# Kernel optimization log

Hardware: AMD Instinct MI355X
Metric: run time of the kernel (lower is better)

## Reference

```python
import jax, jax.numpy as jnp
import numpy as np

N = 50000      # num_nodes
E = 800000     # num_edges
D = 128        # hidden_dim
POOL_RATIO = 0.5
CROSS_W = 1.0  # cross_weight


def _gcn(x, W, b, src, dst, n):
    """GCNConv: symmetric-normalized aggregation with self-loops. Dropout is identity (eval)."""
    loops = jnp.arange(n)
    s = jnp.concatenate([src, loops])
    d = jnp.concatenate([dst, loops])
    deg = jax.ops.segment_sum(jnp.ones(s.shape, x.dtype), d, num_segments=n)
    inv_sqrt = jax.lax.rsqrt(jnp.maximum(deg, 1.0))  # deg >= 1 due to self-loops
    xw = x @ W                                        # [n, D]
    msg = xw[s] * (inv_sqrt[s] * inv_sqrt[d])[:, None]  # [E+n, D] gather
    return jax.ops.segment_sum(msg, d, num_segments=n) + b


def _prelu(x, a):
    return jnp.where(x >= 0, x, a * x)


def setup_inputs() -> dict:
    key = jax.random.key(0)
    ks = jax.random.split(key, 8)
    glorot = lambda k, sh: jax.random.normal(k, sh, jnp.float32) * np.float32(np.sqrt(2.0 / (sh[0] + sh[1])))
    return {
        "feat": jax.random.normal(ks[0], (N, D), jnp.float32),
        "h_neg": jax.random.normal(ks[1], (N, D), jnp.float32),
        "edge_index": jax.random.randint(ks[2], (2, E), 0, N),
        "Wd": glorot(ks[3], (D, D)),
        "bd": jnp.zeros((D,), jnp.float32),
        "prelu_a": jnp.full((1,), 0.25, jnp.float32),
        "Wbil": glorot(ks[4], (D, D)),
        "bbil": jnp.zeros((1,), jnp.float32),
        "Wg1": glorot(ks[5], (D, D)),
        "bg1": jnp.zeros((D,), jnp.float32),
        "Wg2": glorot(ks[6], (D, D)),
        "bg2": jnp.zeros((D,), jnp.float32),
        "Wg3": glorot(ks[7], (D, D)),
        "bg3": jnp.zeros((D,), jnp.float32),
    }


def reference(feat, h_neg, edge_index, Wd, bd, prelu_a, Wbil, bbil,
              Wg1, bg1, Wg2, bg2, Wg3, bg3):
    src, dst = edge_index[0], edge_index[1]
    # --- IndexSelect: dense layer on pos/neg features ---
    h_pos = _prelu(feat @ Wd + bd, prelu_a)
    h_neg_d = _prelu(h_neg @ Wd + bd, prelu_a)
    embed = _gcn(h_pos, Wg1, bg1, src, dst, N)
    h_center = jax.nn.sigmoid(embed)
    # Discriminator (bilinear) positive scores -> node importance
    score_pos = jnp.einsum('nd,de,ne->n', h_pos, Wbil, h_center) + bbil[0]
    _ = jnp.einsum('nd,de,ne->n', h_neg_d, Wbil, h_center) + bbil[0]  # score_neg (logits branch)
    scores = jax.nn.sigmoid(score_pos)
    order = jnp.argsort(-scores)           # descending
    k = int(POOL_RATIO * N)
    select_idx = order[:k]
    select_scores = scores[order][:k]
    # --- GraphPool (use_gcn=True): down-sample GCN, gather, scale ---
    pooled = _gcn(embed, Wg2, bg2, src, dst, N)[select_idx] * select_scores[:, None]
    # --- GraphUnpool: scatter into zeros, up-sample GCN ---
    fine = jnp.zeros((N, D), feat.dtype).at[select_idx].set(pooled)
    out = _gcn(fine, Wg3, bg3, src, dst, N)
    # --- cross/fuse connection ---
    return out + CROSS_W * embed
```

## Files before the change

### kernel.cpp

```cpp
#include <hip/hip_runtime.h>
#include <hip/hip_bf16.h>

#define NN 50000
#define NE 800000
#define DD 128
#define KSEL 25000
#define NBK 391
#define NBLKA 98
#define AB 12500

typedef unsigned int uint32;
typedef unsigned short ushort16;
typedef __attribute__((ext_vector_type(8))) short bf16x8;
typedef __attribute__((ext_vector_type(4))) float f32x4;

__device__ __forceinline__ float sigmoidf(float x){ return 1.f/(1.f+__expf(-x)); }

__device__ __forceinline__ unsigned short f2b(float f){
  union{float f; unsigned u;} v; v.f=f;
  unsigned r=(v.u + 0x7fffu + ((v.u>>16)&1u))>>16;
  return (unsigned short)r;
}

__device__ __forceinline__ void addbf2(float&lo,float&hi,uint32 u,float w){
  lo+=__uint_as_float(u<<16)*w;
  hi+=__uint_as_float(u&0xffff0000u)*w;
}

__device__ __forceinline__ int aload(const int* p){
  return __hip_atomic_load(p,__ATOMIC_RELAXED,__HIP_MEMORY_SCOPE_AGENT);
}

__global__ __launch_bounds__(256) void k_prep(const float* __restrict__ Wbil,
    float* __restrict__ WbT, const float* __restrict__ Wg2, ushort16* __restrict__ Wt2b,
    const float* __restrict__ Wg3, ushort16* __restrict__ Wt3b,
    int* __restrict__ zspan, int* __restrict__ btot){
  int i=blockIdx.x*256+threadIdx.x;
  if(i<DD*DD){
    int n=i>>7, k=i&127;
    WbT[i]=Wbil[k*DD+n];
    Wt2b[i]=f2b(Wg2[(size_t)k*DD+n]);
    Wt3b[i]=f2b(Wg3[(size_t)k*DD+n]);
  }
  if(i<8512) zspan[i]=0;
  if(i<NBK) btot[i]=0;
}

__global__ __launch_bounds__(1024) void k_bcount(const int* __restrict__ dst,
    int* __restrict__ btot, int* __restrict__ blkcnt){
  __shared__ int h[NBK];
  int tid=threadIdx.x;
  for(int i=tid;i<NBK;i+=1024) h[i]=0;
  __syncthreads();
  int e0=blockIdx.x*8192;
  #pragma unroll
  for(int t=0;t<8;t++){
    int e=e0+t*1024+tid;
    if(e<NE) atomicAdd(&h[dst[e]>>7],1);
  }
  __syncthreads();
  for(int i=tid;i<NBK;i+=1024){
    int c=h[i];
    blkcnt[blockIdx.x*NBK+i]=c;
    if(c) atomicAdd(&btot[i],c);
  }
}

__global__ __launch_bounds__(512) void k_bscan(const int* __restrict__ btot,
    int* __restrict__ boff, const int* __restrict__ blkcnt, int* __restrict__ blkbase,
    int* __restrict__ row_start){
  __shared__ int sdata[512];
  int tid=threadIdx.x;
  int v=(tid<NBK)?btot[tid]:0;
  sdata[tid]=v; __syncthreads();
  for(int off=1;off<512;off<<=1){
    int y=(tid>=off)?sdata[tid-off]:0;
    __syncthreads();
    sdata[tid]+=y;
    __syncthreads();
  }
  int excl=sdata[tid]-v;
  if(tid<NBK) boff[tid]=excl;
  if(tid==NBK-1){ boff[NBK]=excl+v; row_start[NN]=NE; }
  if(tid<NBK){
    int run=excl;
    for(int b=0;b<NBLKA;b++){
      int c=blkcnt[b*NBK+tid];
      blkbase[b*NBK+tid]=run;
      run+=c;
    }
  }
}

__global__ __launch_bounds__(1024) void k_bscatter(const int* __restrict__ src,
    const int* __restrict__ dst, const int* __restrict__ blkbase, uint32* __restrict__ pairs){
  __shared__ int cur[NBK];
  int tid=threadIdx.x;
  for(int i=tid;i<NBK;i+=1024) cur[i]=blkbase[blockIdx.x*NBK+i];
  __syncthreads();
  int e0=blockIdx.x*8192;
  #pragma unroll
  for(int t=0;t<8;t++){
    int e=e0+t*1024+tid;
    if(e<NE){
      int d=dst[e];
      int p=atomicAdd(&cur[d>>7],1);
      pairs[p]=(unsigned)src[e] | ((unsigned)(d&127)<<17);
    }
  }
}

__global__ __launch_bounds__(256) void k_bfinal(const uint32* __restrict__ pairs,
    const int* __restrict__ boff, int* __restrict__ row_start,
    float* __restrict__ inv_sq, int* __restrict__ csr_src){
  __shared__ int degl[128];
  __shared__ int cur[128];
  __shared__ int ssum[2];
  int b=blockIdx.x, tid=threadIdx.x;
  int lo=boff[b], hi=boff[b+1];
  if(tid<128) degl[tid]=0;
  __syncthreads();
  for(int e=lo+tid;e<hi;e+=256) atomicAdd(&degl[pairs[e]>>17],1);
  __syncthreads();
  int v=0,x=0;
  if(tid<128){
    v=degl[tid]; x=v;
    #pragma unroll
    for(int off=1;off<64;off<<=1){
      int y=__shfl_up(x,off,64);
      if((tid&63)>=off) x+=y;
    }
    if((tid&63)==63) ssum[tid>>6]=x;
  }
  __syncthreads();
  if(tid<128){
    int incl=x+((tid>=64)?ssum[0]:0);
    int node=b*128+tid;
    int excl=lo+incl-v;
    if(node<NN){
      row_start[node]=excl;
      cur[tid]=excl;
      inv_sq[node]=1.f/sqrtf((float)(v+1));
    }
  }
  __syncthreads();
  for(int e=lo+tid;e<hi;e+=256){
    uint32 u=pairs[e];
    int p=atomicAdd(&cur[u>>17],1);
    csr_src[p]=(int)(u&0x1FFFFu);
  }
}

template<int IN_SIG,int ACT,int FUSE_SCORE>
__global__ __launch_bounds__(256) void k_gemm64t(const float* __restrict__ A,
    const float* __restrict__ W, const float* __restrict__ bias,
    float* __restrict__ outf,
    const float* __restrict__ aparam, const float* __restrict__ hp,
    const float* __restrict__ bbil, float* __restrict__ score){
  __shared__ float Al[64][132];
  int tid=threadIdx.x;
  int row0=blockIdx.x*64;
  {
    const float4* A4=(const float4*)(A+(size_t)row0*DD);
    #pragma unroll
    for(int i=0;i<8;i++){
      int idx=i*256+tid;
      int r=idx>>5, c=(idx&31)*4;
      float4 v=make_float4(0.f,0.f,0.f,0.f);
      if(row0+r<NN) v=A4[idx];
      if(IN_SIG){ v.x=sigmoidf(v.x); v.y=sigmoidf(v.y); v.z=sigmoidf(v.z); v.w=sigmoidf(v.w); }
      *(float4*)&Al[r][c]=v;
    }
  }
  __syncthreads();
  int tx=tid&31, ty=tid>>5;
  float acc[8][4];
  #pragma unroll
  for(int i=0;i<8;i++)
    #pragma unroll
    for(int c=0;c<4;c++) acc[i][c]=0.f;

  for(int k=0;k<DD;k+=4){
    float4 wv0=*(const float4*)&W[(size_t)(k+0)*DD+tx*4];
    float4 wv1=*(const float4*)&W[(size_t)(k+1)*DD+tx*4];
    float4 wv2=*(const float4*)&W[(size_t)(k+2)*DD+tx*4];
    float4 wv3=*(const float4*)&W[(size_t)(k+3)*DD+tx*4];
    #pragma unroll
    for(int i=0;i<8;i++){
      float4 a=*(const float4*)&Al[ty+8*i][k];
      acc[i][0]+=a.x*wv0.x+a.y*wv1.x+a.z*wv2.x+a.w*wv3.x;
      acc[i][1]+=a.x*wv0.y+a.y*wv1.y+a.z*wv2.y+a.w*wv3.y;
      acc[i][2]+=a.x*wv0.z+a.y*wv1.z+a.z*wv2.z+a.w*wv3.z;
      acc[i][3]+=a.x*wv0.w+a.y*wv1.w+a.z*wv2.w+a.w*wv3.w;
    }
  }

  if(FUSE_SCORE){
    float bb=bbil[0];
    #pragma unroll
    for(int i=0;i<8;i++){
      int r=row0+ty+8*i;
      float p=0.f;
      if(r<NN){
        float4 h=*(const float4*)&hp[(size_t)r*DD+tx*4];
        p=acc[i][0]*h.x+acc[i][1]*h.y+acc[i][2]*h.z+acc[i][3]*h.w;
      }
      p+=__shfl_xor(p,16,64); p+=__shfl_xor(p,8,64);
      p+=__shfl_xor(p,4,64);  p+=__shfl_xor(p,2,64); p+=__shfl_xor(p,1,64);
      if(tx==0 && r<NN) score[r]=sigmoidf(p+bb);
    }
    return;
  }
  float4 bv=make_float4(0.f,0.f,0.f,0.f);
  if(bias) bv=*(const float4*)&bias[tx*4];
  float ap=ACT?aparam[0]:0.f;
  #pragma unroll
  for(int i=0;i<8;i++){
    int r=row0+ty+8*i;
    if(r<NN){
      float4 o;
      o.x=acc[i][0]+bv.x; o.y=acc[i][1]+bv.y; o.z=acc[i][2]+bv.z; o.w=acc[i][3]+bv.w;
      if(ACT){
        o.x=o.x>=0.f?o.x:ap*o.x; o.y=o.y>=0.f?o.y:ap*o.y;
        o.z=o.z>=0.f?o.z:ap*o.z; o.w=o.w>=0.f?o.w:ap*o.w;
      }
      *(float4*)&outf[(size_t)r*DD+tx*4]=o;
    }
  }
}

template<int ROWLIST>
__global__ __launch_bounds__(256) void k_gemm_mfma(const float* __restrict__ A,
    const ushort16* __restrict__ Wtb, ushort16* __restrict__ outb,
    const int* __restrict__ rlist){
  __shared__ __align__(16) unsigned short Asl[64][136];
  __shared__ __align__(16) unsigned short Wsl[128][136];
  int tid=threadIdx.x;
  int row0=blockIdx.x*64;
  {
    const uint4* Wg=(const uint4*)Wtb;
    #pragma unroll
    for(int i=0;i<8;i++){
      int idx=i*256+tid;
      int n=idx>>4, k8=(idx&15)*8;
      uint4 v=Wg[idx];
      *(uint4*)&Wsl[n][k8]=v;
    }
  }
  {
    #pragma unroll
    for(int i=0;i<8;i++){
      int idx=i*256+tid;
      int r=idx>>5, c=(idx&31)*4;
      int gr; bool ok;
      if(ROWLIST){ int ri=row0+r; ok=(ri<KSEL); gr=ok?rlist[ri]:0; }
      else { gr=row0+r; ok=(gr<NN); }
      float4 v=make_float4(0.f,0.f,0.f,0.f);
      if(ok) v=*(const float4*)&A[(size_t)gr*DD+c];
      ushort4 pk;
      pk.x=f2b(v.x); pk.y=f2b(v.y); pk.z=f2b(v.z); pk.w=f2b(v.w);
      *(ushort4*)&Asl[r][c]=pk;
    }
  }
  __syncthreads();
  int lane=tid&63, w=tid>>6;
  int lr=lane&15, lk=lane>>4;
  f32x4 acc[8];
  #pragma unroll
  for(int nf=0;nf<8;nf++){ acc[nf][0]=0.f; acc[nf][1]=0.f; acc[nf][2]=0.f; acc[nf][3]=0.f; }
  #pragma unroll
  for(int kk=0;kk<4;kk++){
    int k0=kk*32+lk*8;
    bf16x8 a=*(bf16x8*)&Asl[w*16+lr][k0];
    #pragma unroll
    for(int nf=0;nf<8;nf++){
      bf16x8 b=*(bf16x8*)&Wsl[nf*16+lr][k0];
      acc[nf]=__builtin_amdgcn_mfma_f32_16x16x32_bf16(a,b,acc[nf],0,0,0);
    }
  }
  int orow[4]; bool ok[4];
  #pragma unroll
  for(int i=0;i<4;i++){
    int ri=row0+w*16+lk*4+i;
    if(ROWLIST){ ok[i]=(ri<KSEL); orow[i]=ok[i]?rlist[ri]:0; }
    else { orow[i]=ri; ok[i]=(ri<NN); }
  }
  #pragma unroll
  for(int nf=0;nf<8;nf++){
    int col=nf*16+lr;
    #pragma unroll
    for(int i=0;i<4;i++){
      if(ok[i]) outb[(size_t)orow[i]*DD+col]=f2b(acc[nf][i]);
    }
  }
}

__global__ __launch_bounds__(256) void k_agg_f32(const float* __restrict__ xw,
    const int* __restrict__ row_start, const int* __restrict__ csr,
    const float* __restrict__ inv, const float* __restrict__ bias,
    float* __restrict__ outp){
  int node=blockIdx.x*4+(threadIdx.x>>6);
  if(node>=NN) return;
  int lane=threadIdx.x&63;
  int g=lane>>5, li=lane&31;
  int rs=row_start[node], re=row_start[node+1];
  float a0=0.f,a1=0.f,a2=0.f,a3=0.f;
  int j=rs;
  for(; j+7<re; j+=8){
    int s0=csr[j+g], s1=csr[j+2+g], s2=csr[j+4+g], s3=csr[j+6+g];
    float w0=inv[s0], w1=inv[s1], w2=inv[s2], w3=inv[s3];
    float4 v0=*(const float4*)&xw[(size_t)s0*DD+li*4];
    float4 v1=*(const float4*)&xw[(size_t)s1*DD+li*4];
    float4 v2=*(const float4*)&xw[(size_t)s2*DD+li*4];
    float4 v3=*(const float4*)&xw[(size_t)s3*DD+li*4];
    a0+=v0.x*w0+v1.x*w1+v2.x*w2+v3.x*w3;
    a1+=v0.y*w0+v1.y*w1+v2.y*w2+v3.y*w3;
    a2+=v0.z*w0+v1.z*w1+v2.z*w2+v3.z*w3;
    a3+=v0.w*w0+v1.w*w1+v2.w*w2+v3.w*w3;
  }
  for(; j+1<re; j+=2){
    int s=csr[j+g];
    float w=inv[s];
    float4 v=*(const float4*)&xw[(size_t)s*DD+li*4];
    a0+=v.x*w; a1+=v.y*w; a2+=v.z*w; a3+=v.w*w;
  }
  if(j<re && g==0){
    int s=csr[j]; float w=inv[s];
    float4 v=*(const float4*)&xw[(size_t)s*DD+li*4];
    a0+=v.x*w; a1+=v.y*w; a2+=v.z*w; a3+=v.w*w;
  }
  if(g==0){
    float wd=inv[node];
    float4 v=*(const float4*)&xw[(size_t)node*DD+li*4];
    a0+=v.x*wd; a1+=v.y*wd; a2+=v.z*wd; a3+=v.w*wd;
  }
  a0+=__shfl_xor(a0,32,64); a1+=__shfl_xor(a1,32,64);
  a2+=__shfl_xor(a2,32,64); a3+=__shfl_xor(a3,32,64);
  if(g==0){
    float wn=inv[node];
    float4 bv=*(const float4*)&bias[li*4];
    float4 o;
    o.x=a0*wn+bv.x; o.y=a1*wn+bv.y; o.z=a2*wn+bv.z; o.w=a3*wn+bv.w;
    *(float4*)&outp[(size_t)node*DD+li*4]=o;
  }
}

template<int MODE>
__global__ __launch_bounds__(256) void k_agg_b16(const uint32* __restrict__ xwb,
    const int* __restrict__ row_start, const int* __restrict__ csr,
    const float* __restrict__ inv, const float* __restrict__ bias,
    float* __restrict__ outp, const float* __restrict__ score,
    const unsigned char* __restrict__ sel, const float* __restrict__ addbuf,
    const int* __restrict__ list){
  int idx4=blockIdx.x*4+(threadIdx.x>>6);
  int node;
  if(MODE==1){ if(idx4>=KSEL) return; node=list[idx4]; }
  else { node=idx4; if(node>=NN) return; }
  int lane=threadIdx.x&63;
  int g=lane>>4, li=lane&15;
  int rs=row_start[node], re=row_start[node+1];
  float a[8];
  #pragma unroll
  for(int c=0;c<8;c++) a[c]=0.f;
  int j=rs;
  for(; j+7<re; j+=8){
    int sA=csr[j+g], sB=csr[j+4+g];
    if(MODE!=2 || sel[sA]){
      float w=inv[sA];
      uint4 u=*(const uint4*)(xwb+(size_t)sA*64+li*4);
      addbf2(a[0],a[1],u.x,w); addbf2(a[2],a[3],u.y,w);
      addbf2(a[4],a[5],u.z,w); addbf2(a[6],a[7],u.w,w);
    }
    if(MODE!=2 || sel[sB]){
      float w=inv[sB];
      uint4 u=*(const uint4*)(xwb+(size_t)sB*64+li*4);
      addbf2(a[0],a[1],u.x,w); addbf2(a[2],a[3],u.y,w);
      addbf2(a[4],a[5],u.z,w); addbf2(a[6],a[7],u.w,w);
    }
  }
  for(; j+3<re; j+=4){
    int s=csr[j+g];
    if(MODE!=2 || sel[s]){
      float w=inv[s];
      uint4 u=*(const uint4*)(xwb+(size_t)s*64+li*4);
      addbf2(a[0],a[1],u.x,w); addbf2(a[2],a[3],u.y,w);
      addbf2(a[4],a[5],u.z,w); addbf2(a[6],a[7],u.w,w);
    }
  }
  int rem=re-j;
  if(g<rem){
    int s=csr[j+g];
    if(MODE!=2 || sel[s]){
      float w=inv[s];
      uint4 u=*(const uint4*)(xwb+(size_t)s*64+li*4);
      addbf2(a[0],a[1],u.x,w); addbf2(a[2],a[3],u.y,w);
      addbf2(a[4],a[5],u.z,w); addbf2(a[6],a[7],u.w,w);
    }
  }
  if(g==0 && (MODE!=2 || sel[node])){
    float wd=inv[node];
    uint4 u=*(const uint4*)(xwb+(size_t)node*64+li*4);
    addbf2(a[0],a[1],u.x,wd); addbf2(a[2],a[3],u.y,wd);
    addbf2(a[4],a[5],u.z,wd); addbf2(a[6],a[7],u.w,wd);
  }
  #pragma unroll
  for(int c=0;c<8;c++){
    a[c]+=__shfl_xor(a[c],16,64);
    a[c]+=__shfl_xor(a[c],32,64);
  }
  if(g<2){
    float wn=inv[node];
    int cb=li*8+g*4;
    float4 bv=*(const float4*)&bias[cb];
    float r0=a[g*4+0]*wn+bv.x, r1=a[g*4+1]*wn+bv.y;
    float r2=a[g*4+2]*wn+bv.z, r3=a[g*4+3]*wn+bv.w;
    if(MODE==1){
      float sc=score[node];
      r0*=sc; r1*=sc; r2*=sc; r3*=sc;
    } else {
      float4 ad=*(const float4*)&addbuf[(size_t)node*DD+cb];
      r0+=ad.x; r1+=ad.y; r2+=ad.z; r3+=ad.w;
    }
    float4 o; o.x=r0; o.y=r1; o.z=r2; o.w=r3;
    *(float4*)&outp[(size_t)node*DD+cb]=o;
  }
}

template<int NB,int PASS>
__global__ __launch_bounds__(256) void k_hist(const float* __restrict__ score,
    int* __restrict__ ghist, int* __restrict__ ctrl){
  __shared__ int lh[NB];
  __shared__ int gs[256];
  __shared__ int lastf;
  int tid=threadIdx.x;
  for(int i=tid;i<NB;i+=256) lh[i]=0;
  __syncthreads();
  int p0=0,p01=0;
  if(PASS==1) p0=ctrl[0];
  if(PASS==2) p01=ctrl[2];
  for(int i=blockIdx.x*256+tid; i<NN; i+=gridDim.x*256){
    unsigned b=__float_as_uint(score[i]);
    if(PASS==0) atomicAdd(&lh[b>>20],1);
    else if(PASS==1){ if((int)(b>>20)==p0) atomicAdd(&lh[(b>>8)&0xFFF],1); }
    else { if((int)(b>>8)==p01) atomicAdd(&lh[b&0xFF],1); }
  }
  __syncthreads();
  for(int i=tid;i<NB;i+=256){ int v=lh[i]; if(v) atomicAdd(&ghist[i],v); }
  __syncthreads();
  if(tid==0){
    __threadfence();
    int v=atomicAdd(&ctrl[8+PASS],1);
    lastf=(v==(int)gridDim.x-1);
  }
  __syncthreads();
  if(!lastf) return;
  const int BPT=NB/256;
  int s=0;
  #pragma unroll
  for(int q=0;q<BPT;q++) s+=aload(&ghist[tid*BPT+q]);
  int x=s; gs[tid]=x; __syncthreads();
  for(int off=1;off<256;off<<=1){
    int y=(tid+off<256)?gs[tid+off]:0;
    __syncthreads(); x+=y; gs[tid]=x; __syncthreads();
  }
  int base;
  if(PASS==0) base=0; else if(PASS==1) base=ctrl[1]; else base=ctrl[3];
  int above=base+x-s, incl=base+x;
  if(above<KSEL && incl>=KSEL){
    int c=above, B=0;
    for(int b=BPT-1;b>=0;b--){
      int hb=aload(&ghist[tid*BPT+b]);
      if(c+hb>=KSEL){ B=tid*BPT+b; break; }
      c+=hb;
    }
    if(PASS==0){ ctrl[0]=B; ctrl[1]=c; }
    else if(PASS==1){ ctrl[2]=(ctrl[0]<<12)|B; ctrl[3]=c; }
    else { ctrl[4]=(int)((((unsigned)ctrl[2])<<8)|(unsigned)B); ctrl[5]=KSEL-c; }
  }
}

__global__ __launch_bounds__(256) void k_sel(const float* __restrict__ score,
    int* __restrict__ ctrl, int* __restrict__ tie_list,
    unsigned char* __restrict__ sel, int* __restrict__ list){
  __shared__ int lastf;
  int tid=threadIdx.x;
  int i=blockIdx.x*256+tid;
  if(i<NN){
    unsigned b=__float_as_uint(score[i]);
    unsigned thr=(unsigned)ctrl[4];
    if(b>thr){
      sel[i]=1;
      int p=atomicAdd(&ctrl[7],1);
      list[p]=i;
    } else if(b==thr){
      sel[i]=0;
      int p=atomicAdd(&ctrl[6],1);
      if(p<4096) __hip_atomic_store(&tie_list[p],i,__ATOMIC_RELAXED,__HIP_MEMORY_SCOPE_AGENT);
    } else sel[i]=0;
  }
  __syncthreads();
  if(tid==0){
    __threadfence();
    int v=atomicAdd(&ctrl[11],1);
    lastf=(v==(int)gridDim.x-1);
  }
  __syncthreads();
  if(!lastf) return;
  int m=aload(&ctrl[6]); if(m>4096) m=4096;
  int needed=ctrl[5];
  for(int t=tid;t<m;t+=256){
    int idx=aload(&tie_list[t]);
    int rank=0;
    for(int j2=0;j2<m;j2++) rank+=(aload(&tie_list[j2])<idx)?1:0;
    if(rank<needed){
      sel[idx]=1;
      int p=atomicAdd(&ctrl[7],1);
      list[p]=idx;
    }
  }
}

extern "C" void kernel_launch(void* const* d_in, const int* in_sizes, int n_in,
                              void* d_out, int out_size, void* d_ws, size_t ws_size,
                              hipStream_t stream){
  const float* feat   =(const float*)d_in[0];
  const int*   ei     =(const int*)  d_in[2];
  const int*   src    = ei;
  const int*   dst    = ei + NE;
  const float* Wd     =(const float*)d_in[3];
  const float* bd     =(const float*)d_in[4];
  const float* prelu_a=(const float*)d_in[5];
  const float* Wbil   =(const float*)d_in[6];
  const float* bbil   =(const float*)d_in[7];
  const float* Wg1    =(const float*)d_in[8];
  const float* bg1    =(const float*)d_in[9];
  const float* Wg2    =(const float*)d_in[10];
  const float* bg2    =(const float*)d_in[11];
  const float* Wg3    =(const float*)d_in[12];
  const float* bg3    =(const float*)d_in[13];
  float* out=(float*)d_out;

  char* p=(char*)d_ws;
  auto alloc=[&](size_t bytes)->void*{ void* r=(void*)p; p+=((bytes+255)/256)*256; return r; };
  float* h_pos   =(float*)alloc((size_t)NN*DD*4);
  float* embed   =(float*)alloc((size_t)NN*DD*4);
  float* xw      =(float*)alloc((size_t)NN*DD*4);
  float* score   =(float*)alloc((size_t)NN*4);
  float* inv_sq  =(float*)alloc((size_t)NN*4);
  float* WbT     =(float*)alloc((size_t)DD*DD*4);
  ushort16* Wt2b =(ushort16*)alloc((size_t)DD*DD*2);
  ushort16* Wt3b =(ushort16*)alloc((size_t)DD*DD*2);
  int*   row_st  =(int*)  alloc((size_t)(NN+1)*4);
  int*   csr_src =(int*)  alloc((size_t)NE*4);
  int*   ctrl    =(int*)  alloc(256);
  int*   hist0   =(int*)  alloc(4096*4);
  int*   hist1   =(int*)  alloc(4096*4);
  int*   hist2   =(int*)  alloc(256*4);
  int*   tie_list=(int*)  alloc(4096*4);
  int*   list    =(int*)  alloc((size_t)KSEL*4);
  unsigned char* sel=(unsigned char*)alloc(NN);
  int*   btot    =(int*)  alloc((size_t)NBK*4);
  int*   boff    =(int*)  alloc((size_t)(NBK+1)*4);
  int*   blkcnt  =(int*)  alloc((size_t)NBLKA*NBK*4);
  int*   blkbase =(int*)  alloc((size_t)NBLKA*NBK*4);
  uint32* pairs  =(uint32*)xw;
  ushort16* xwb  =(ushort16*)xw;
  float* fine = out;

  const int NB=(NN+255)/256;
  const int GB=(NN+63)/64;
  const int GBL=(KSEL+63)/64;
  const int ABL=(KSEL+3)/4;

  k_prep<<<64,256,0,stream>>>(Wbil, WbT, Wg2, Wt2b, Wg3, Wt3b, ctrl, btot);

  k_bcount  <<<NBLKA,1024,0,stream>>>(dst, btot, blkcnt);
  k_bscan   <<<1,512,0,stream>>>(btot, boff, blkcnt, blkbase, row_st);
  k_bscatter<<<NBLKA,1024,0,stream>>>(src, dst, blkbase, pairs);
  k_bfinal  <<<NBK,256,0,stream>>>(pairs, boff, row_st, inv_sq, csr_src);

  k_gemm64t<0,1,0><<<GB,256,0,stream>>>(feat, Wd, bd, h_pos, prelu_a, nullptr, nullptr, nullptr);
  k_gemm64t<0,0,0><<<GB,256,0,stream>>>(h_pos, Wg1, nullptr, xw, nullptr, nullptr, nullptr, nullptr);
  k_agg_f32<<<AB,256,0,stream>>>(xw, row_st, csr_src, inv_sq, bg1, embed);
  k_gemm64t<1,0,1><<<GB,256,0,stream>>>(embed, WbT, nullptr, nullptr, nullptr, h_pos, bbil, score);
  k_hist<4096,0><<<64,256,0,stream>>>(score, hist0, ctrl);
  k_hist<4096,1><<<64,256,0,stream>>>(score, hist1, ctrl);
  k_hist<256,2><<<64,256,0,stream>>>(score, hist2, ctrl);
  k_sel<<<NB,256,0,stream>>>(score, ctrl, tie_list, sel, list);
  k_gemm_mfma<0><<<GB,256,0,stream>>>(embed, Wt2b, xwb, nullptr);
  k_agg_b16<1><<<ABL,256,0,stream>>>((const uint32*)xwb, row_st, csr_src, inv_sq, bg2, fine, score, sel, nullptr, list);
  k_gemm_mfma<1><<<GBL,256,0,stream>>>(fine, Wt3b, xwb, list);
  k_agg_b16<2><<<AB,256,0,stream>>>((const uint32*)xwb, row_st, csr_src, inv_sq, bg3, out, nullptr, sel, embed, nullptr);
}
```

Measured before the change: 330.0 us.

## Pack independent kernels into shared launches to cut launch count

Merges independent work into single heterogeneous launches by block index: the dense layer, the CSR bucket count and the weight prep share one grid, the Wg1 GEMM shares a grid with the bucket scan, and the Wg2 MFMA GEMM shares a grid with the first score-histogram pass. This is meant to cut kernel-launch and tail idle time on a mostly serial chain of small kernels and to let latency-bound CSR work overlap the GEMMs. The bucket-count grid is widened to more smaller blocks, and the scan becomes a single block with long serial loops over many block counts, which may end up on the critical path. The pairs buffer moves from xw to embed so the scatter does not clash with the concurrent GEMM output.

```diff
diff --git a/kernel.cpp b/kernel.cpp
--- a/kernel.cpp
+++ b/kernel.cpp
@@ -6,8 +6,11 @@
 #define DD 128
 #define KSEL 25000
 #define NBK 391
-#define NBLKA 98
+#define BC  391
 #define AB 12500
+#define GB 782
+#define GBL 391
+#define HB 64
 
 typedef unsigned int uint32;
 typedef unsigned short ushort16;
@@ -31,135 +34,11 @@
   return __hip_atomic_load(p,__ATOMIC_RELAXED,__HIP_MEMORY_SCOPE_AGENT);
 }
 
-__global__ __launch_bounds__(256) void k_prep(const float* __restrict__ Wbil,
-    float* __restrict__ WbT, const float* __restrict__ Wg2, ushort16* __restrict__ Wt2b,
-    const float* __restrict__ Wg3, ushort16* __restrict__ Wt3b,
-    int* __restrict__ zspan, int* __restrict__ btot){
-  int i=blockIdx.x*256+threadIdx.x;
-  if(i<DD*DD){
-    int n=i>>7, k=i&127;
-    WbT[i]=Wbil[k*DD+n];
-    Wt2b[i]=f2b(Wg2[(size_t)k*DD+n]);
-    Wt3b[i]=f2b(Wg3[(size_t)k*DD+n]);
-  }
-  if(i<8512) zspan[i]=0;
-  if(i<NBK) btot[i]=0;
-}
-
-__global__ __launch_bounds__(1024) void k_bcount(const int* __restrict__ dst,
-    int* __restrict__ btot, int* __restrict__ blkcnt){
-  __shared__ int h[NBK];
-  int tid=threadIdx.x;
-  for(int i=tid;i<NBK;i+=1024) h[i]=0;
-  __syncthreads();
-  int e0=blockIdx.x*8192;
-  #pragma unroll
-  for(int t=0;t<8;t++){
-    int e=e0+t*1024+tid;
-    if(e<NE) atomicAdd(&h[dst[e]>>7],1);
-  }
-  __syncthreads();
-  for(int i=tid;i<NBK;i+=1024){
-    int c=h[i];
-    blkcnt[blockIdx.x*NBK+i]=c;
-    if(c) atomicAdd(&btot[i],c);
-  }
-}
-
-__global__ __launch_bounds__(512) void k_bscan(const int* __restrict__ btot,
-    int* __restrict__ boff, const int* __restrict__ blkcnt, int* __restrict__ blkbase,
-    int* __restrict__ row_start){
-  __shared__ int sdata[512];
-  int tid=threadIdx.x;
-  int v=(tid<NBK)?btot[tid]:0;
-  sdata[tid]=v; __syncthreads();
-  for(int off=1;off<512;off<<=1){
-    int y=(tid>=off)?sdata[tid-off]:0;
-    __syncthreads();
-    sdata[tid]+=y;
-    __syncthreads();
-  }
-  int excl=sdata[tid]-v;
-  if(tid<NBK) boff[tid]=excl;
-  if(tid==NBK-1){ boff[NBK]=excl+v; row_start[NN]=NE; }
-  if(tid<NBK){
-    int run=excl;
-    for(int b=0;b<NBLKA;b++){
-      int c=blkcnt[b*NBK+tid];
-      blkbase[b*NBK+tid]=run;
-      run+=c;
-    }
-  }
-}
-
-__global__ __launch_bounds__(1024) void k_bscatter(const int* __restrict__ src,
-    const int* __restrict__ dst, const int* __restrict__ blkbase, uint32* __restrict__ pairs){
-  __shared__ int cur[NBK];
-  int tid=threadIdx.x;
-  for(int i=tid;i<NBK;i+=1024) cur[i]=blkbase[blockIdx.x*NBK+i];
-  __syncthreads();
-  int e0=blockIdx.x*8192;
-  #pragma unroll
-  for(int t=0;t<8;t++){
-    int e=e0+t*1024+tid;
-    if(e<NE){
-      int d=dst[e];
-      int p=atomicAdd(&cur[d>>7],1);
-      pairs[p]=(unsigned)src[e] | ((unsigned)(d&127)<<17);
-    }
-  }
-}
-
-__global__ __launch_bounds__(256) void k_bfinal(const uint32* __restrict__ pairs,
-    const int* __restrict__ boff, int* __restrict__ row_start,
-    float* __restrict__ inv_sq, int* __restrict__ csr_src){
-  __shared__ int degl[128];
-  __shared__ int cur[128];
-  __shared__ int ssum[2];
-  int b=blockIdx.x, tid=threadIdx.x;
-  int lo=boff[b], hi=boff[b+1];
-  if(tid<128) degl[tid]=0;
-  __syncthreads();
-  for(int e=lo+tid;e<hi;e+=256) atomicAdd(&degl[pairs[e]>>17],1);
-  __syncthreads();
-  int v=0,x=0;
-  if(tid<128){
-    v=degl[tid]; x=v;
-    #pragma unroll
-    for(int off=1;off<64;off<<=1){
-      int y=__shfl_up(x,off,64);
-      if((tid&63)>=off) x+=y;
-    }
-    if((tid&63)==63) ssum[tid>>6]=x;
-  }
-  __syncthreads();
-  if(tid<128){
-    int incl=x+((tid>=64)?ssum[0]:0);
-    int node=b*128+tid;
-    int excl=lo+incl-v;
-    if(node<NN){
-      row_start[node]=excl;
-      cur[tid]=excl;
-      inv_sq[node]=1.f/sqrtf((float)(v+1));
-    }
-  }
-  __syncthreads();
-  for(int e=lo+tid;e<hi;e+=256){
-    uint32 u=pairs[e];
-    int p=atomicAdd(&cur[u>>17],1);
-    csr_src[p]=(int)(u&0x1FFFFu);
-  }
-}
-
-template<int IN_SIG,int ACT,int FUSE_SCORE>
-__global__ __launch_bounds__(256) void k_gemm64t(const float* __restrict__ A,
-    const float* __restrict__ W, const float* __restrict__ bias,
-    float* __restrict__ outf,
-    const float* __restrict__ aparam, const float* __restrict__ hp,
-    const float* __restrict__ bbil, float* __restrict__ score){
-  __shared__ float Al[64][132];
-  int tid=threadIdx.x;
-  int row0=blockIdx.x*64;
+template<int IN_SIG,int ACT>
+__device__ __forceinline__ void gemm64_body(float (*Al)[132], int tid, int row0,
+    const float* __restrict__ A, const float* __restrict__ W,
+    const float* __restrict__ bias, float* __restrict__ outf,
+    const float* __restrict__ aparam){
   {
     const float4* A4=(const float4*)(A+(size_t)row0*DD);
     #pragma unroll
@@ -179,7 +58,6 @@
   for(int i=0;i<8;i++)
     #pragma unroll
     for(int c=0;c<4;c++) acc[i][c]=0.f;
-
   for(int k=0;k<DD;k+=4){
     float4 wv0=*(const float4*)&W[(size_t)(k+0)*DD+tx*4];
     float4 wv1=*(const float4*)&W[(size_t)(k+1)*DD+tx*4];
@@ -193,23 +71,6 @@
       acc[i][2]+=a.x*wv0.z+a.y*wv1.z+a.z*wv2.z+a.w*wv3.z;
       acc[i][3]+=a.x*wv0.w+a.y*wv1.w+a.z*wv2.w+a.w*wv3.w;
     }
-  }
-
-  if(FUSE_SCORE){
-    float bb=bbil[0];
-    #pragma unroll
-    for(int i=0;i<8;i++){
-      int r=row0+ty+8*i;
-      float p=0.f;
-      if(r<NN){
-        float4 h=*(const float4*)&hp[(size_t)r*DD+tx*4];
-        p=acc[i][0]*h.x+acc[i][1]*h.y+acc[i][2]*h.z+acc[i][3]*h.w;
-      }
-      p+=__shfl_xor(p,16,64); p+=__shfl_xor(p,8,64);
-      p+=__shfl_xor(p,4,64);  p+=__shfl_xor(p,2,64); p+=__shfl_xor(p,1,64);
-      if(tx==0 && r<NN) score[r]=sigmoidf(p+bb);
-    }
-    return;
   }
   float4 bv=make_float4(0.f,0.f,0.f,0.f);
   if(bias) bv=*(const float4*)&bias[tx*4];
@@ -230,13 +91,10 @@
 }
 
 template<int ROWLIST>
-__global__ __launch_bounds__(256) void k_gemm_mfma(const float* __restrict__ A,
-    const ushort16* __restrict__ Wtb, ushort16* __restrict__ outb,
-    const int* __restrict__ rlist){
-  __shared__ __align__(16) unsigned short Asl[64][136];
-  __shared__ __align__(16) unsigned short Wsl[128][136];
-  int tid=threadIdx.x;
-  int row0=blockIdx.x*64;
+__device__ __forceinline__ void mfma_body(unsigned short (*Asl)[136],
+    unsigned short (*Wsl)[136], int tid, int row0,
+    const float* __restrict__ A, const ushort16* __restrict__ Wtb,
+    ushort16* __restrict__ outb, const int* __restrict__ rlist){
   {
     const uint4* Wg=(const uint4*)Wtb;
     #pragma unroll
@@ -293,6 +151,356 @@
       if(ok[i]) outb[(size_t)orow[i]*DD+col]=f2b(acc[nf][i]);
     }
   }
+}
+
+__global__ __launch_bounds__(256) void k_pack1(
+    const float* __restrict__ feat, const float* __restrict__ Wd,
+    const float* __restrict__ bd, float* __restrict__ h_pos,
+    const float* __restrict__ aparam,
+    const int* __restrict__ dst, int* __restrict__ blkcnt,
+    const float* __restrict__ Wbil, float* __restrict__ WbT,
+    const float* __restrict__ Wg2, ushort16* __restrict__ Wt2b,
+    const float* __restrict__ Wg3, ushort16* __restrict__ Wt3b,
+    int* __restrict__ zspan){
+  __shared__ float Al[64][132];
+  int bid=blockIdx.x, tid=threadIdx.x;
+  if(bid<GB){
+    gemm64_body<0,1>(Al, tid, bid*64, feat, Wd, bd, h_pos, aparam);
+    return;
+  }
+  if(bid<GB+BC){
+    int b=bid-GB;
+    int* h=(int*)Al;
+    for(int i=tid;i<NBK;i+=256) h[i]=0;
+    __syncthreads();
+    int e0=b*2048;
+    #pragma unroll
+    for(int t=0;t<8;t++){
+      int e=e0+t*256+tid;
+      if(e<NE) atomicAdd(&h[dst[e]>>7],1);
+    }
+    __syncthreads();
+    for(int i=tid;i<NBK;i+=256) blkcnt[b*NBK+i]=h[i];
+    return;
+  }
+  int i=(bid-GB-BC)*256+tid;
+  if(i<DD*DD){
+    int n=i>>7, k=i&127;
+    WbT[i]=Wbil[k*DD+n];
+    Wt2b[i]=f2b(Wg2[(size_t)k*DD+n]);
+    Wt3b[i]=f2b(Wg3[(size_t)k*DD+n]);
+  }
+  if(i<8512) zspan[i]=0;
+}
+
+__global__ __launch_bounds__(256) void k_pack2(
+    const float* __restrict__ h_pos, const float* __restrict__ Wg1,
+    float* __restrict__ xw,
+    const int* __restrict__ blkcnt, int* __restrict__ boff,
+    int* __restrict__ blkbase, int* __restrict__ row_start){
+  __shared__ float Al[64][132];
+  int bid=blockIdx.x, tid=threadIdx.x;
+  if(bid<GB){
+    gemm64_body<0,0>(Al, tid, bid*64, h_pos, Wg1, nullptr, xw, nullptr);
+    return;
+  }
+  int* sd=(int*)Al;
+  int b0=tid, b1=tid+256;
+  int s0=0, s1=0;
+  for(int b=0;b<BC;b++){
+    s0+=blkcnt[b*NBK+b0];
+    if(b1<NBK) s1+=blkcnt[b*NBK+b1];
+  }
+  sd[b0]=s0; sd[b1]=(b1<NBK)?s1:0;
+  __syncthreads();
+  for(int off=1;off<512;off<<=1){
+    int a0=(b0>=off)?sd[b0-off]:0;
+    int a1=(b1>=off)?sd[b1-off]:0;
+    __syncthreads();
+    sd[b0]+=a0; sd[b1]+=a1;
+    __syncthreads();
+  }
+  int excl0=sd[b0]-s0;
+  boff[b0]=excl0;
+  int excl1=0;
+  if(b1<NBK){ excl1=sd[b1]-s1; boff[b1]=excl1; }
+  if(tid==0){ boff[NBK]=NE; row_start[NN]=NE; }
+  {
+    int run=excl0;
+    for(int b=0;b<BC;b++){
+      int c=blkcnt[b*NBK+b0];
+      blkbase[b*NBK+b0]=run;
+      run+=c;
+    }
+  }
+  if(b1<NBK){
+    int run=excl1;
+    for(int b=0;b<BC;b++){
+      int c=blkcnt[b*NBK+b1];
+      blkbase[b*NBK+b1]=run;
+      run+=c;
+    }
+  }
+}
+
+__global__ __launch_bounds__(256) void k_bscatter(const int* __restrict__ src,
+    const int* __restrict__ dst, const int* __restrict__ blkbase, uint32* __restrict__ pairs){
+  __shared__ int cur[NBK];
+  int tid=threadIdx.x, b=blockIdx.x;
+  for(int i=tid;i<NBK;i+=256) cur[i]=blkbase[b*NBK+i];
+  __syncthreads();
+  int e0=b*2048;
+  #pragma unroll
+  for(int t=0;t<8;t++){
+    int e=e0+t*256+tid;
+    if(e<NE){
+      int d=dst[e];
+      int p=atomicAdd(&cur[d>>7],1);
+      pairs[p]=(unsigned)src[e] | ((unsigned)(d&127)<<17);
+    }
+  }
+}
+
+__global__ __launch_bounds__(256) void k_bfinal(const uint32* __restrict__ pairs,
+    const int* __restrict__ boff, int* __restrict__ row_start,
+    float* __restrict__ inv_sq, int* __restrict__ csr_src){
+  __shared__ int degl[128];
+  __shared__ int cur[128];
+  __shared__ int ssum[2];
+  int b=blockIdx.x, tid=threadIdx.x;
+  int lo=boff[b], hi=boff[b+1];
+  if(tid<128) degl[tid]=0;
+  __syncthreads();
+  for(int e=lo+tid;e<hi;e+=256) atomicAdd(&degl[pairs[e]>>17],1);
+  __syncthreads();
+  int v=0,x=0;
+  if(tid<128){
+    v=degl[tid]; x=v;
+    #pragma unroll
+    for(int off=1;off<64;off<<=1){
+      int y=__shfl_up(x,off,64);
+      if((tid&63)>=off) x+=y;
+    }
+    if((tid&63)==63) ssum[tid>>6]=x;
+  }
+  __syncthreads();
+  if(tid<128){
+    int incl=x+((tid>=64)?ssum[0]:0);
+    int node=b*128+tid;
+    int excl=lo+incl-v;
+    if(node<NN){
+      row_start[node]=excl;
+      cur[tid]=excl;
+      inv_sq[node]=1.f/sqrtf((float)(v+1));
+    }
+  }
+  __syncthreads();
+  for(int e=lo+tid;e<hi;e+=256){
+    uint32 u=pairs[e];
+    int p=atomicAdd(&cur[u>>17],1);
+    csr_src[p]=(int)(u&0x1FFFFu);
+  }
+}
+
+__global__ __launch_bounds__(256) void k_gemm_score(const float* __restrict__ A,
+    const float* __restrict__ W, const float* __restrict__ hp,
+    const float* __restrict__ bbil, float* __restrict__ score){
+  __shared__ float Al[64][132];
+  int tid=threadIdx.x;
+  int row0=blockIdx.x*64;
+  {
+    const float4* A4=(const float4*)(A+(size_t)row0*DD);
+    #pragma unroll
+    for(int i=0;i<8;i++){
+      int idx=i*256+tid;
+      int r=idx>>5, c=(idx&31)*4;
+      float4 v=make_float4(0.f,0.f,0.f,0.f);
+      if(row0+r<NN) v=A4[idx];
+      v.x=sigmoidf(v.x); v.y=sigmoidf(v.y); v.z=sigmoidf(v.z); v.w=sigmoidf(v.w);
+      *(float4*)&Al[r][c]=v;
+    }
+  }
+  __syncthreads();
+  int tx=tid&31, ty=tid>>5;
+  float acc[8][4];
+  #pragma unroll
+  for(int i=0;i<8;i++)
+    #pragma unroll
+    for(int c=0;c<4;c++) acc[i][c]=0.f;
+  for(int k=0;k<DD;k+=4){
+    float4 wv0=*(const float4*)&W[(size_t)(k+0)*DD+tx*4];
+    float4 wv1=*(const float4*)&W[(size_t)(k+1)*DD+tx*4];
+    float4 wv2=*(const float4*)&W[(size_t)(k+2)*DD+tx*4];
+    float4 wv3=*(const float4*)&W[(size_t)(k+3)*DD+tx*4];
+    #pragma unroll
+    for(int i=0;i<8;i++){
+      float4 a=*(const float4*)&Al[ty+8*i][k];
+      acc[i][0]+=a.x*wv0.x+a.y*wv1.x+a.z*wv2.x+a.w*wv3.x;
+      acc[i][1]+=a.x*wv0.y+a.y*wv1.y+a.z*wv2.y+a.w*wv3.y;
+      acc[i][2]+=a.x*wv0.z+a.y*wv1.z+a.z*wv2.z+a.w*wv3.z;
+      acc[i][3]+=a.x*wv0.w+a.y*wv1.w+a.z*wv2.w+a.w*wv3.w;
+    }
+  }
+  float bb=bbil[0];
+  #pragma unroll
+  for(int i=0;i<8;i++){
+    int r=row0+ty+8*i;
+    float p=0.f;
+    if(r<NN){
+      float4 h=*(const float4*)&hp[(size_t)r*DD+tx*4];
+      p=acc[i][0]*h.x+acc[i][1]*h.y+acc[i][2]*h.z+acc[i][3]*h.w;
+    }
+    p+=__shfl_xor(p,16,64); p+=__shfl_xor(p,8,64);
+    p+=__shfl_xor(p,4,64);  p+=__shfl_xor(p,2,64); p+=__shfl_xor(p,1,64);
+    if(tx==0 && r<NN) score[r]=sigmoidf(p+bb);
+  }
+}
+
+__global__ __launch_bounds__(256) void k_pack3(const float* __restrict__ embed,
+    const ushort16* __restrict__ Wt2b, ushort16* __restrict__ outb,
+    const float* __restrict__ score, int* __restrict__ ghist, int* __restrict__ ctrl){
+  __shared__ __align__(16) unsigned short Asl[64][136];
+  __shared__ __align__(16) unsigned short Wsl[128][136];
+  __shared__ int lastf;
+  int bid=blockIdx.x, tid=threadIdx.x;
+  if(bid<GB){
+    mfma_body<0>(Asl, Wsl, tid, bid*64, embed, Wt2b, outb, nullptr);
+    return;
+  }
+  int hb=bid-GB;
+  int* lh=(int*)Asl;
+  int* gs=(int*)Wsl;
+  for(int i=tid;i<4096;i+=256) lh[i]=0;
+  __syncthreads();
+  for(int i=hb*256+tid;i<NN;i+=HB*256)
+    atomicAdd(&lh[__float_as_uint(score[i])>>20],1);
+  __syncthreads();
+  for(int i=tid;i<4096;i+=256){ int v=lh[i]; if(v) atomicAdd(&ghist[i],v); }
+  __syncthreads();
+  if(tid==0){
+    __threadfence();
+    int v=atomicAdd(&ctrl[8],1);
+    lastf=(v==HB-1);
+  }
+  __syncthreads();
+  if(!lastf) return;
+  int s=0;
+  #pragma unroll
+  for(int q=0;q<16;q++) s+=aload(&ghist[tid*16+q]);
+  int x=s; gs[tid]=x; __syncthreads();
+  for(int off=1;off<256;off<<=1){
+    int y=(tid+off<256)?gs[tid+off]:0;
+    __syncthreads(); x+=y; gs[tid]=x; __syncthreads();
+  }
+  int above=x-s, incl=x;
+  if(above<KSEL && incl>=KSEL){
+    int c=above, B=0;
+    for(int b=15;b>=0;b--){
+      int hb2=aload(&ghist[tid*16+b]);
+      if(c+hb2>=KSEL){ B=tid*16+b; break; }
+      c+=hb2;
+    }
+    ctrl[0]=B; ctrl[1]=c;
+  }
+}
+
+template<int NB,int PASS>
+__global__ __launch_bounds__(256) void k_hist(const float* __restrict__ score,
+    int* __restrict__ ghist, int* __restrict__ ctrl){
+  __shared__ int lh[NB];
+  __shared__ int gs[256];
+  __shared__ int lastf;
+  int tid=threadIdx.x;
+  for(int i=tid;i<NB;i+=256) lh[i]=0;
+  __syncthreads();
+  int p0=0,p01=0;
+  if(PASS==1) p0=ctrl[0];
+  if(PASS==2) p01=ctrl[2];
+  for(int i=blockIdx.x*256+tid; i<NN; i+=gridDim.x*256){
+    unsigned b=__float_as_uint(score[i]);
+    if(PASS==1){ if((int)(b>>20)==p0) atomicAdd(&lh[(b>>8)&0xFFF],1); }
+    else { if((int)(b>>8)==p01) atomicAdd(&lh[b&0xFF],1); }
+  }
+  __syncthreads();
+  for(int i=tid;i<NB;i+=256){ int v=lh[i]; if(v) atomicAdd(&ghist[i],v); }
+  __syncthreads();
+  if(tid==0){
+    __threadfence();
+    int v=atomicAdd(&ctrl[8+PASS],1);
+    lastf=(v==(int)gridDim.x-1);
+  }
+  __syncthreads();
+  if(!lastf) return;
+  const int BPT=NB/256;
+  int s=0;
+  #pragma unroll
+  for(int q=0;q<BPT;q++) s+=aload(&ghist[tid*BPT+q]);
+  int x=s; gs[tid]=x; __syncthreads();
+  for(int off=1;off<256;off<<=1){
+    int y=(tid+off<256)?gs[tid+off]:0;
+    __syncthreads(); x+=y; gs[tid]=x; __syncthreads();
+  }
+  int base=(PASS==1)?ctrl[1]:ctrl[3];
+  int above=base+x-s, incl=base+x;
+  if(above<KSEL && incl>=KSEL){
+    int c=above, B=0;
+    for(int b=BPT-1;b>=0;b--){
+      int hb=aload(&ghist[tid*BPT+b]);
+      if(c+hb>=KSEL){ B=tid*BPT+b; break; }
+      c+=hb;
+    }
+    if(PASS==1){ ctrl[2]=(ctrl[0]<<12)|B; ctrl[3]=c; }
+    else { ctrl[4]=(int)((((unsigned)ctrl[2])<<8)|(unsigned)B); ctrl[5]=KSEL-c; }
+  }
+}
+
+__global__ __launch_bounds__(256) void k_sel(const float* __restrict__ score,
+    int* __restrict__ ctrl, int* __restrict__ tie_list,
+    unsigned char* __restrict__ sel, int* __restrict__ list){
+  __shared__ int lastf;
+  int tid=threadIdx.x;
+  int i=blockIdx.x*256+tid;
+  if(i<NN){
+    unsigned b=__float_as_uint(score[i]);
+    unsigned thr=(unsigned)ctrl[4];
+    if(b>thr){
+      sel[i]=1;
+      int p=atomicAdd(&ctrl[7],1);
+      list[p]=i;
+    } else if(b==thr){
+      sel[i]=0;
+      int p=atomicAdd(&ctrl[6],1);
+      if(p<4096) __hip_atomic_store(&tie_list[p],i,__ATOMIC_RELAXED,__HIP_MEMORY_SCOPE_AGENT);
+    } else sel[i]=0;
+  }
+  __syncthreads();
+  if(tid==0){
+    __threadfence();
+    int v=atomicAdd(&ctrl[11],1);
+    lastf=(v==(int)gridDim.x-1);
+  }
+  __syncthreads();
+  if(!lastf) return;
+  int m=aload(&ctrl[6]); if(m>4096) m=4096;
+  int needed=ctrl[5];
+  for(int t=tid;t<m;t+=256){
+    int idx=aload(&tie_list[t]);
+    int rank=0;
+    for(int j2=0;j2<m;j2++) rank+=(aload(&tie_list[j2])<idx)?1:0;
+    if(rank<needed){
+      sel[idx]=1;
+      int p=atomicAdd(&ctrl[7],1);
+      list[p]=idx;
+    }
+  }
+}
+
+__global__ __launch_bounds__(256) void k_gemm_mfma1(const float* __restrict__ A,
+    const ushort16* __restrict__ Wtb, ushort16* __restrict__ outb,
+    const int* __restrict__ rlist){
+  __shared__ __align__(16) unsigned short Asl[64][136];
+  __shared__ __align__(16) unsigned short Wsl[128][136];
+  mfma_body<1>(Asl, Wsl, threadIdx.x, blockIdx.x*64, A, Wtb, outb, rlist);
 }
 
 __global__ __launch_bounds__(256) void k_agg_f32(const float* __restrict__ xw,
@@ -426,100 +634,6 @@
   }
 }
 
-template<int NB,int PASS>
-__global__ __launch_bounds__(256) void k_hist(const float* __restrict__ score,
-    int* __restrict__ ghist, int* __restrict__ ctrl){
-  __shared__ int lh[NB];
-  __shared__ int gs[256];
-  __shared__ int lastf;
-  int tid=threadIdx.x;
-  for(int i=tid;i<NB;i+=256) lh[i]=0;
-  __syncthreads();
-  int p0=0,p01=0;
-  if(PASS==1) p0=ctrl[0];
-  if(PASS==2) p01=ctrl[2];
-  for(int i=blockIdx.x*256+tid; i<NN; i+=gridDim.x*256){
-    unsigned b=__float_as_uint(score[i]);
-    if(PASS==0) atomicAdd(&lh[b>>20],1);
-    else if(PASS==1){ if((int)(b>>20)==p0) atomicAdd(&lh[(b>>8)&0xFFF],1); }
-    else { if((int)(b>>8)==p01) atomicAdd(&lh[b&0xFF],1); }
-  }
-  __syncthreads();
-  for(int i=tid;i<NB;i+=256){ int v=lh[i]; if(v) atomicAdd(&ghist[i],v); }
-  __syncthreads();
-  if(tid==0){
-    __threadfence();
-    int v=atomicAdd(&ctrl[8+PASS],1);
-    lastf=(v==(int)gridDim.x-1);
-  }
-  __syncthreads();
-  if(!lastf) return;
-  const int BPT=NB/256;
-  int s=0;
-  #pragma unroll
-  for(int q=0;q<BPT;q++) s+=aload(&ghist[tid*BPT+q]);
-  int x=s; gs[tid]=x; __syncthreads();
-  for(int off=1;off<256;off<<=1){
-    int y=(tid+off<256)?gs[tid+off]:0;
-    __syncthreads(); x+=y; gs[tid]=x; __syncthreads();
-  }
-  int base;
-  if(PASS==0) base=0; else if(PASS==1) base=ctrl[1]; else base=ctrl[3];
-  int above=base+x-s, incl=base+x;
-  if(above<KSEL && incl>=KSEL){
-    int c=above, B=0;
-    for(int b=BPT-1;b>=0;b--){
-      int hb=aload(&ghist[tid*BPT+b]);
-      if(c+hb>=KSEL){ B=tid*BPT+b; break; }
-      c+=hb;
-    }
-    if(PASS==0){ ctrl[0]=B; ctrl[1]=c; }
-    else if(PASS==1){ ctrl[2]=(ctrl[0]<<12)|B; ctrl[3]=c; }
-    else { ctrl[4]=(int)((((unsigned)ctrl[2])<<8)|(unsigned)B); ctrl[5]=KSEL-c; }
-  }
-}
-
-__global__ __launch_bounds__(256) void k_sel(const float* __restrict__ score,
-    int* __restrict__ ctrl, int* __restrict__ tie_list,
-    unsigned char* __restrict__ sel, int* __restrict__ list){
-  __shared__ int lastf;
-  int tid=threadIdx.x;
-  int i=blockIdx.x*256+tid;
-  if(i<NN){
-    unsigned b=__float_as_uint(score[i]);
-    unsigned thr=(unsigned)ctrl[4];
-    if(b>thr){
-      sel[i]=1;
-      int p=atomicAdd(&ctrl[7],1);
-      list[p]=i;
-    } else if(b==thr){
-      sel[i]=0;
-      int p=atomicAdd(&ctrl[6],1);
-      if(p<4096) __hip_atomic_store(&tie_list[p],i,__ATOMIC_RELAXED,__HIP_MEMORY_SCOPE_AGENT);
-    } else sel[i]=0;
-  }
-  __syncthreads();
-  if(tid==0){
-    __threadfence();
-    int v=atomicAdd(&ctrl[11],1);
-    lastf=(v==(int)gridDim.x-1);
-  }
-  __syncthreads();
-  if(!lastf) return;
-  int m=aload(&ctrl[6]); if(m>4096) m=4096;
-  int needed=ctrl[5];
-  for(int t=tid;t<m;t+=256){
-    int idx=aload(&tie_list[t]);
-    int rank=0;
-    for(int j2=0;j2<m;j2++) rank+=(aload(&tie_list[j2])<idx)?1:0;
-    if(rank<needed){
-      sel[idx]=1;
-      int p=atomicAdd(&ctrl[7],1);
-      list[p]=idx;
-    }
-  }
-}
-
 extern "C" void kernel_launch(void* const* d_in, const int* in_sizes, int n_in,
                               void* d_out, int out_size, void* d_ws, size_t ws_size,
                               hipStream_t stream){
@@ -559,36 +673,28 @@
   int*   tie_list=(int*)  alloc(4096*4);
   int*   list    =(int*)  alloc((size_t)KSEL*4);
   unsigned char* sel=(unsigned char*)alloc(NN);
-  int*   btot    =(int*)  alloc((size_t)NBK*4);
   int*   boff    =(int*)  alloc((size_t)(NBK+1)*4);
-  int*   blkcnt  =(int*)  alloc((size_t)NBLKA*NBK*4);
-  int*   blkbase =(int*)  alloc((size_t)NBLKA*NBK*4);
-  uint32* pairs  =(uint32*)xw;
+  int*   blkcnt  =(int*)  alloc((size_t)BC*NBK*4);
+  int*   blkbase =(int*)  alloc((size_t)BC*NBK*4);
+  uint32* pairs  =(uint32*)embed;
   ushort16* xwb  =(ushort16*)xw;
   float* fine = out;
 
   const int NB=(NN+255)/256;
-  const int GB=(NN+63)/64;
-  const int GBL=(KSEL+63)/64;
   const int ABL=(KSEL+3)/4;
 
-  k_prep<<<64,256,0,stream>>>(Wbil, WbT, Wg2, Wt2b, Wg3, Wt3b, ctrl, btot);
-
-  k_bcount  <<<NBLKA,1024,0,stream>>>(dst, btot, blkcnt);
-  k_bscan   <<<1,512,0,stream>>>(btot, boff, blkcnt, blkbase, row_st);
-  k_bscatter<<<NBLKA,1024,0,stream>>>(src, dst, blkbase, pairs);
-  k_bfinal  <<<NBK,256,0,stream>>>(pairs, boff, row_st, inv_sq, csr_src);
-
-  k_gemm64t<0,1,0><<<GB,256,0,stream>>>(feat, Wd, bd, h_pos, prelu_a, nullptr, nullptr, nullptr);
-  k_gemm64t<0,0,0><<<GB,256,0,stream>>>(h_pos, Wg1, nullptr, xw, nullptr, nullptr, nullptr, nullptr);
+  k_pack1<<<GB+BC+64,256,0,stream>>>(feat, Wd, bd, h_pos, prelu_a,
+      dst, blkcnt, Wbil, WbT, Wg2, Wt2b, Wg3, Wt3b, ctrl);
+  k_pack2<<<GB+1,256,0,stream>>>(h_pos, Wg1, xw, blkcnt, boff, blkbase, row_st);
+  k_bscatter<<<BC,256,0,stream>>>(src, dst, blkbase, pairs);
+  k_bfinal  <<<BC,256,0,stream>>>(pairs, boff, row_st, inv_sq, csr_src);
   k_agg_f32<<<AB,256,0,stream>>>(xw, row_st, csr_src, inv_sq, bg1, embed);
-  k_gemm64t<1,0,1><<<GB,256,0,stream>>>(embed, WbT, nullptr, nullptr, nullptr, h_pos, bbil, score);
-  k_hist<4096,0><<<64,256,0,stream>>>(score, hist0, ctrl);
-  k_hist<4096,1><<<64,256,0,stream>>>(score, hist1, ctrl);
-  k_hist<256,2><<<64,256,0,stream>>>(score, hist2, ctrl);
+  k_gemm_score<<<GB,256,0,stream>>>(embed, WbT, h_pos, bbil, score);
+  k_pack3<<<GB+HB,256,0,stream>>>(embed, Wt2b, xwb, score, hist0, ctrl);
+  k_hist<4096,1><<<HB,256,0,stream>>>(score, hist1, ctrl);
+  k_hist<256,2><<<HB,256,0,stream>>>(score, hist2, ctrl);
   k_sel<<<NB,256,0,stream>>>(score, ctrl, tie_list, sel, list);
-  k_gemm_mfma<0><<<GB,256,0,stream>>>(embed, Wt2b, xwb, nullptr);
   k_agg_b16<1><<<ABL,256,0,stream>>>((const uint32*)xwb, row_st, csr_src, inv_sq, bg2, fine, score, sel, nullptr, list);
-  k_gemm_mfma<1><<<GBL,256,0,stream>>>(fine, Wt3b, xwb, list);
+  k_gemm_mfma1<<<GBL,256,0,stream>>>(fine, Wt3b, xwb, list);
   k_agg_b16<2><<<AB,256,0,stream>>>((const uint32*)xwb, row_st, csr_src, inv_sq, bg3, out, nullptr, sel, embed, nullptr);
 }
```

After: 427.2 us. 1.29x slower.
